# Optimization experiments

Hardware: AMD Instinct MI355X
Metric: run time of the kernel (lower is better)

The kernel has to match this reference:

```python
import math
import jax, jax.numpy as jnp
import numpy as np

B, T, C = 2, 2048, 1024
H, N1, N2, N3 = 16, 6, 4, 6
HD = C // H  # 64


def setup_inputs() -> dict:
    key = jax.random.key(0)
    k1, k2, k3 = jax.random.split(key, 3)
    return {
        "x": jax.random.normal(k1, (B, T, C), jnp.float32),
        "qkv_w": jax.random.normal(k2, (3 * C, C), jnp.float32) * (C ** -0.5),
        "proj_w": jax.random.normal(k3, (C, C), jnp.float32) * (C ** -0.5),
        "proj_b": jnp.zeros((C,), jnp.float32),
        "curvature": jnp.ones((1, N2, 1, 1), jnp.float32),
    }


def _rotary(T_, hd, dtype):
    inv_freq = 1.0 / (10000.0 ** (jnp.arange(0, hd, 2, dtype=jnp.float32) / hd))
    freqs = jnp.outer(jnp.arange(T_, dtype=jnp.float32), inv_freq)  # [T, hd/2]
    return jnp.cos(freqs)[None, :, None, :].astype(dtype), jnp.sin(freqs)[None, :, None, :].astype(dtype)


def _apply_rot(x, cos, sin):
    x1, x2 = x[..., : x.shape[-1] // 2], x[..., x.shape[-1] // 2 :]
    return jnp.concatenate([x1 * cos + x2 * sin, -x1 * sin + x2 * cos], axis=-1).astype(x.dtype)


def _causal_bias(L, S, dtype):
    mask = jnp.triu(jnp.ones((L, S), bool), k=1)
    return jnp.where(mask, jnp.asarray(-jnp.inf, dtype), jnp.asarray(0.0, dtype))


def _sdpa(q, k, v, scale):
    # q,k,v: [B,h,T,hd]
    scores = jnp.einsum("bhtd,bhsd->bhts", q, k) * scale + _causal_bias(q.shape[-2], k.shape[-2], q.dtype)
    return jnp.einsum("bhts,bhsd->bhtd", jax.nn.softmax(scores, axis=-1), v)


def _hyp_attn(q, k, v, curv):
    # Lorentz-model hyperbolic attention. project(x,k) = [sqrt(1/k+||x||^2), x];
    # d(u,v) = sqrt(1/k) * arccosh(-k * <u,v>_L), <u,v>_L = -u0 v0 + <u_s, v_s>.
    eps = 1e-6
    tq = jnp.sqrt(1.0 / curv + jnp.sum(q * q, axis=-1, keepdims=True))  # [B,h,T,1]
    tk = jnp.sqrt(1.0 / curv + jnp.sum(k * k, axis=-1, keepdims=True))  # [B,h,S,1]
    inner = jnp.einsum("bhtd,bhsd->bhts", q, k) - tq * jnp.swapaxes(tk, -1, -2)  # Lorentz inner [B,h,T,S]
    arg = jnp.maximum(-curv * inner, 1.0 + 1e-7)
    dis = jnp.sqrt(1.0 / curv) * jnp.arccosh(arg)
    scores = 1.0 / (eps + dis) + _causal_bias(q.shape[-2], k.shape[-2], q.dtype)
    return jnp.einsum("bhts,bhsd->bhtd", jax.nn.softmax(scores, axis=-1), v)


def reference(x, qkv_w, proj_w, proj_b, curvature):
    Bx, Tx, Cx = x.shape
    qkv = x @ qkv_w.T  # [B,T,3C]
    q, k, v = jnp.split(qkv, 3, axis=-1)
    q = q.reshape(Bx, Tx, H, HD)
    k = k.reshape(Bx, Tx, H, HD)
    v = v.reshape(Bx, Tx, H, HD)
    cos, sin = _rotary(Tx, HD, x.dtype)
    q = _apply_rot(q, cos, sin)
    k = _apply_rot(k, cos, sin)
    # -> [B,H,T,hd]
    q, k, v = (jnp.swapaxes(t, 1, 2) for t in (q, k, v))
    outs = []
    # euclidean heads
    outs.append(_sdpa(q[:, :N1], k[:, :N1], v[:, :N1], 1.0 / math.sqrt(HD)))
    # hyperbolic heads
    outs.append(_hyp_attn(q[:, N1 : N1 + N2], k[:, N1 : N1 + N2], v[:, N1 : N1 + N2], curvature))
    # spherical heads (cosine-sim attention, scale = sqrt(head_dim))
    qn = q[:, N1 + N2 :] / jnp.maximum(jnp.linalg.norm(q[:, N1 + N2 :], axis=-1, keepdims=True), 1e-12)
    kn = k[:, N1 + N2 :] / jnp.maximum(jnp.linalg.norm(k[:, N1 + N2 :], axis=-1, keepdims=True), 1e-12)
    outs.append(_sdpa(qn, kn, v[:, N1 + N2 :], math.sqrt(HD)))
    y = jnp.concatenate(outs, axis=1)  # [B,H,T,hd]
    y = jnp.swapaxes(y, 1, 2).reshape(Bx, Tx, Cx)
    return y @ proj_w.T + proj_b
```

## Files before the change

### kernel.cpp

```cpp
#include <hip/hip_runtime.h>
#include <stdint.h>
#include <math.h>


typedef __bf16 bf16x8 __attribute__((ext_vector_type(8)));
typedef float f32x4 __attribute__((ext_vector_type(4)));

static __device__ __forceinline__ float bf2f(unsigned short u) {
  union { unsigned int i; float f; } v; v.i = ((unsigned int)u) << 16; return v.f;
}
static __device__ __forceinline__ unsigned short f2bf(float f) {
  union { float f; unsigned int i; } v; v.f = f;
  unsigned int x = v.i;
  x += 0x7fffu + ((x >> 16) & 1u);
  return (unsigned short)(x >> 16);
}

static __device__ __forceinline__ void async_copy16(const void* gsrc, void* ldst) {
  auto* lp = reinterpret_cast<__attribute__((address_space(3))) unsigned int*>(
      reinterpret_cast<uintptr_t>(ldst));
  auto* gp = reinterpret_cast<const __attribute__((address_space(1))) unsigned int*>(
      reinterpret_cast<uintptr_t>(gsrc));
  __builtin_amdgcn_global_load_lds(gp, lp, 16, 0, 0);
}

template <int PAT>
__global__ __launch_bounds__(256) void split2(const float* __restrict__ in,
                                              unsigned short* __restrict__ out) {
  const int row = blockIdx.x;
  const int kq = threadIdx.x * 4;
  const f32x4 x = *(const f32x4*)(in + (size_t)row * 1024 + kq);
  unsigned short hi[4], lo[4];
#pragma unroll
  for (int i = 0; i < 4; ++i) {
    hi[i] = f2bf(x[i]);
    lo[i] = f2bf(x[i] - bf2f(hi[i]));
  }
  uint2 uh, ul;
  uh.x = (unsigned)hi[0] | ((unsigned)hi[1] << 16);
  uh.y = (unsigned)hi[2] | ((unsigned)hi[3] << 16);
  ul.x = (unsigned)lo[0] | ((unsigned)lo[1] << 16);
  ul.y = (unsigned)lo[2] | ((unsigned)lo[3] << 16);
  unsigned short* op = out + (size_t)row * 2048 + kq;
  *(uint2*)(op)        = uh;
  *(uint2*)(op + 1024) = PAT ? uh : ul;
}

__global__ __launch_bounds__(256) void split1(const float* __restrict__ in,
                                              unsigned short* __restrict__ out) {
  const int row = blockIdx.x;
  const int kq = threadIdx.x * 4;
  const f32x4 x = *(const f32x4*)(in + (size_t)row * 1024 + kq);
  uint2 uh;
  uh.x = (unsigned)f2bf(x[0]) | ((unsigned)f2bf(x[1]) << 16);
  uh.y = (unsigned)f2bf(x[2]) | ((unsigned)f2bf(x[3]) << 16);
  *(uint2*)(out + (size_t)row * 1024 + kq) = uh;
}

template <int HASBIAS>
__global__ __launch_bounds__(256) void gemm_bt2(
    const unsigned short* __restrict__ A, const unsigned short* __restrict__ Bm,
    float* __restrict__ C, const float* __restrict__ bias,
    int NX, int N_, int Kr, int loN) {
  alignas(16) __shared__ unsigned short smAh[128 * 64];
  alignas(16) __shared__ unsigned short smAl[128 * 64];
  alignas(16) __shared__ unsigned short smB [128 * 64];
  const int tid = threadIdx.x;
  const int lane = tid & 63;
  const int wvi = tid >> 6;
  const int wm = wvi >> 1, wn = wvi & 1;
  const int cpx = gridDim.x >> 3;
  const int wgid = ((int)blockIdx.x & 7) * cpx + ((int)blockIdx.x >> 3);
  const long m0 = (long)(wgid / NX) * 128, n0 = (long)(wgid % NX) * 128;
  const int K2w = Kr * 2;
  const bool skiplo = (n0 >= (long)loN);

  const f32x4 zero4 = {0.f, 0.f, 0.f, 0.f};
  f32x4 acc[4][4];
#pragma unroll
  for (int i = 0; i < 4; ++i)
#pragma unroll
    for (int j = 0; j < 4; ++j) acc[i][j] = zero4;

  int mrow[4], gg[4];
#pragma unroll
  for (int w = 0; w < 4; ++w) {
    int c = w * 256 + tid;
    mrow[w] = c >> 3;
    gg[w] = (c & 7) ^ ((c >> 3) & 7);
  }

  const int kTiles = Kr >> 6;
  for (int kt = 0; kt < kTiles; ++kt) {
    if (kt) __syncthreads();
    const int kb = kt << 6;
#pragma unroll
    for (int w = 0; w < 4; ++w) {
      const int c = w * 256 + tid;
      const size_t arow = (size_t)(m0 + mrow[w]) * K2w + kb + gg[w] * 8;
      async_copy16(A + arow,        (char*)smAh + c * 16);
      if (!skiplo)
        async_copy16(A + arow + Kr, (char*)smAl + c * 16);
      async_copy16(Bm + (size_t)(n0 + mrow[w]) * Kr + kb + gg[w] * 8,
                   (char*)smB + c * 16);
    }
    __syncthreads();
#pragma unroll
    for (int ks = 0; ks < 2; ++ks) {
      bf16x8 afh[4], afl[4], bg[4];
#pragma unroll
      for (int i = 0; i < 4; ++i) {
        const int ra = wm * 64 + i * 16 + (lane & 15);
        const int ga = (ks * 4 + (lane >> 4)) ^ (ra & 7);
        afh[i] = *(const bf16x8*)((const char*)smAh + ra * 128 + ga * 16);
        if (!skiplo)
          afl[i] = *(const bf16x8*)((const char*)smAl + ra * 128 + ga * 16);
        const int rb = wn * 64 + i * 16 + (lane & 15);
        const int gb2 = (ks * 4 + (lane >> 4)) ^ (rb & 7);
        bg[i] = *(const bf16x8*)((const char*)smB + rb * 128 + gb2 * 16);
      }
#pragma unroll
      for (int i = 0; i < 4; ++i)
#pragma unroll
        for (int j = 0; j < 4; ++j) {
          acc[i][j] = __builtin_amdgcn_mfma_f32_16x16x32_bf16(afh[i], bg[j], acc[i][j], 0, 0, 0);
          if (!skiplo)
            acc[i][j] = __builtin_amdgcn_mfma_f32_16x16x32_bf16(afl[i], bg[j], acc[i][j], 0, 0, 0);
        }
    }
  }

  const int r0 = wm * 64 + (lane >> 4) * 4;
  const int c0 = wn * 64 + (lane & 15);
#pragma unroll
  for (int j = 0; j < 4; ++j) {
    const long col = n0 + c0 + j * 16;
    float bv = 0.f;
    if (HASBIAS) bv = bias[col];
#pragma unroll
    for (int i = 0; i < 4; ++i) {
#pragma unroll
      for (int r = 0; r < 4; ++r) {
        const long row = m0 + r0 + i * 16 + r;
        C[row * N_ + col] = acc[i][j][r] + bv;
      }
    }
  }
}

__global__ __launch_bounds__(256) void prep(
    const float* __restrict__ qkvf, unsigned short* __restrict__ Q2,
    unsigned short* __restrict__ K2, unsigned short* __restrict__ V2,
    float* __restrict__ qq, float* __restrict__ kk, const float* __restrict__ curvg) {
  __shared__ unsigned short Vl[64 * 66];
  const int tid = threadIdx.x;
  const int zz = blockIdx.x;
  const int ttile = zz & 31, bh = zz >> 5;
  const int b = bh >> 4, h = bh & 15;
  const int t0 = ttile * 64;
  const int tr = tid >> 2, seg = tid & 3;
  const int t = t0 + tr;
  const float* src = qkvf + ((size_t)(b * 2048 + t)) * 3072 + h * 64 + seg * 16;

  float qv[16], kv[16], vv[16];
#pragma unroll
  for (int c = 0; c < 4; ++c) {
    const f32x4 a  = *(const f32x4*)(src + c * 4);
    const f32x4 bb = *(const f32x4*)(src + 1024 + c * 4);
    const f32x4 cc = *(const f32x4*)(src + 2048 + c * 4);
#pragma unroll
    for (int e = 0; e < 4; ++e) { qv[c*4+e] = a[e]; kv[c*4+e] = bb[e]; vv[c*4+e] = cc[e]; }
  }
  float qr[16], kr[16];
#pragma unroll
  for (int e = 0; e < 16; ++e) {
    const int d = seg * 16 + e;
    const int i = d & 31;
    const float invf = exp2f(-0.41524101186109286f * (float)i);
    float sn, cs;
    sincosf((float)t * invf, &sn, &cs);
    const float qo = __shfl_xor(qv[e], 2, 64);
    const float ko = __shfl_xor(kv[e], 2, 64);
    qr[e] = (d < 32) ? (qv[e] * cs + qo * sn) : (qv[e] * cs - qo * sn);
    kr[e] = (d < 32) ? (kv[e] * cs + ko * sn) : (kv[e] * cs - ko * sn);
  }
  float sq = 0.f, sk = 0.f;
#pragma unroll
  for (int e = 0; e < 16; ++e) { sq += qr[e] * qr[e]; sk += kr[e] * kr[e]; }
  sq += __shfl_xor(sq, 1, 64); sq += __shfl_xor(sq, 2, 64);
  sk += __shfl_xor(sk, 1, 64); sk += __shfl_xor(sk, 2, 64);
  float qscale = 0.125f * 1.4426950408889634f;
  if (h >= 10) {
    const float rq = 1.0f / fmaxf(sqrtf(sq), 1e-12f);
    const float rk = 1.0f / fmaxf(sqrtf(sk), 1e-12f);
#pragma unroll
    for (int e = 0; e < 16; ++e) { qr[e] *= rq; kr[e] *= rk; }
    qscale = 8.0f * 1.4426950408889634f;
  } else if (h >= 6) {
    qscale = 1.0f;
  }
#pragma unroll
  for (int e = 0; e < 16; ++e) qr[e] *= qscale;
  if (seg == 0) {
    const int idx = b * 32768 + h * 2048 + t;
    float oq = sq, ok = sk;
    if (h >= 6 && h < 10) {
      const float invc = 1.0f / curvg[h - 6];
      oq = sqrtf(invc + sq);
      ok = sqrtf(invc + sk);
    }
    qq[idx] = oq;
    kk[idx] = ok;
  }
  const int st = seg >> 1;
  const int quadA = (seg * 2) & 3, quadB = (seg * 2 + 1) & 3;
  {
    unsigned int wh[8], wl[8];
#pragma unroll
    for (int p = 0; p < 8; ++p) {
      unsigned short h0 = f2bf(qr[2*p]), h1 = f2bf(qr[2*p+1]);
      unsigned short l0 = f2bf(qr[2*p] - bf2f(h0)), l1 = f2bf(qr[2*p+1] - bf2f(h1));
      wh[p] = (unsigned)h0 | ((unsigned)h1 << 16);
      wl[p] = (unsigned)l0 | ((unsigned)l1 << 16);
    }
    const int qi = (t >> 4) & 1, c15q = t & 15;
    unsigned short* qs = Q2 + ((size_t)bh * 64 + (t >> 5)) * 4096;
    const int fh = ((qi * 2 + st) * 2 + 0) * 512, fl = fh + 512;
    *(uint4*)(qs + fh + quadA * 128 + c15q * 8) = uint4{wh[0], wh[1], wh[2], wh[3]};
    *(uint4*)(qs + fh + quadB * 128 + c15q * 8) = uint4{wh[4], wh[5], wh[6], wh[7]};
    *(uint4*)(qs + fl + quadA * 128 + c15q * 8) = uint4{wl[0], wl[1], wl[2], wl[3]};
    *(uint4*)(qs + fl + quadB * 128 + c15q * 8) = uint4{wl[4], wl[5], wl[6], wl[7]};
#pragma unroll
    for (int p = 0; p < 8; ++p) {
      unsigned short h0 = f2bf(kr[2*p]), h1 = f2bf(kr[2*p+1]);
      wh[p] = (unsigned)h0 | ((unsigned)h1 << 16);
    }
    const int kj = (tr >> 4) & 3, c15k = tr & 15;
    unsigned short* ks = K2 + ((size_t)bh * 32 + ttile) * 4096;
    const int gh = (st * 4 + kj) * 512;
    *(uint4*)(ks + gh + quadA * 128 + c15k * 8) = uint4{wh[0], wh[1], wh[2], wh[3]};
    *(uint4*)(ks + gh + quadB * 128 + c15k * 8) = uint4{wh[4], wh[5], wh[6], wh[7]};
  }
#pragma unroll
  for (int e = 0; e < 16; ++e) Vl[(seg * 16 + e) * 66 + tr] = f2bf(vv[e]);
  __syncthreads();
  {
    const int d = tid >> 2, tch = (tid & 3) * 16;
    unsigned int wv2[8];
#pragma unroll
    for (int p = 0; p < 8; ++p) {
      const unsigned short a0 = Vl[d * 66 + tch + 2*p];
      const unsigned short a1 = Vl[d * 66 + tch + 2*p + 1];
      wv2[p] = (unsigned)a0 | ((unsigned)a1 << 16);
    }
    const int dj = d >> 4, c15v = d & 15;
    const int ks2 = tch >> 5;
    const int qvA = (tch >> 3) & 3, qvB = ((tch >> 3) + 1) & 3;
    unsigned short* vs = V2 + ((size_t)bh * 32 + ttile) * 4096 + (ks2 * 4 + dj) * 512;
    *(uint4*)(vs + qvA * 128 + c15v * 8) = uint4{wv2[0], wv2[1], wv2[2], wv2[3]};
    *(uint4*)(vs + qvB * 128 + c15v * 8) = uint4{wv2[4], wv2[5], wv2[6], wv2[7]};
  }
}

__global__ __launch_bounds__(256, 2) void attn_part(
    const unsigned short* __restrict__ Q2, const unsigned short* __restrict__ K2,
    const unsigned short* __restrict__ V2, const float* __restrict__ tqq,
    const float* __restrict__ tkk, const float* __restrict__ curvg,
    float* __restrict__ part) {
  const int tid = threadIdx.x;
  const int lane = tid & 63;
  const int wv = tid >> 6;
  const int quad = lane >> 4, c15 = lane & 15;
  const int z = blockIdx.x * 4 + wv;
  const int bh = z / 160;
  const int u = 159 - (z - bh * 160);
  int qw, ch;
  if (u < 16)      { qw = u; ch = 0; }
  else if (u < 48) { qw = 16 + ((u - 16) >> 1); ch = (u - 16) & 1; }
  else if (u < 96) { const int s2 = u - 48; const int q3 = s2 / 3; qw = 32 + q3; ch = s2 - 3 * q3; }
  else             { const int s2 = u - 96; qw = 48 + (s2 >> 2); ch = s2 & 3; }
  const int h = bh & 15;
  const int geom = (h < 6) ? 0 : ((h < 10) ? 1 : 2);
  const int qrow0 = qw * 32;
  const f32x4 zero4 = {0.f, 0.f, 0.f, 0.f};

  const unsigned short* qbase = Q2 + ((size_t)bh * 64 + qw) * 4096;
  bf16x8 qh[2][2], ql[2][2];
#pragma unroll
  for (int qi = 0; qi < 2; ++qi)
#pragma unroll
    for (int st = 0; st < 2; ++st) {
      const int f = ((qi * 2 + st) * 2) * 512 + lane * 8;
      qh[qi][st] = *(const bf16x8*)(qbase + f);
      ql[qi][st] = *(const bf16x8*)(qbase + f + 512);
    }

  float curv = 1.f, sic = 1.f;
  const float Moff = 4.0f;
  float tqs[2] = {0.f, 0.f};
  if (geom == 1) {
    curv = curvg[h - 6];
    sic = sqrtf(1.0f / curv);
#pragma unroll
    for (int qi = 0; qi < 2; ++qi)
      tqs[qi] = tqq[bh * 2048 + qrow0 + qi * 16 + c15];
  }

  const __bf16 one_b = (__bf16)1.0f;
  const bf16x8 ones = {one_b, one_b, one_b, one_b, one_b, one_b, one_b, one_b};

  const int iA = ((quad & 1) * 32 + c15) * 4;
  const int iB = iA + 64;
  const bool hiq = (quad >= 2);

  f32x4 o[2][4];
  f32x4 ol[2] = {zero4, zero4};
#pragma unroll
  for (int qi = 0; qi < 2; ++qi)
#pragma unroll
    for (int dj = 0; dj < 4; ++dj) o[qi][dj] = zero4;

  const int nkt = (qw >> 1) + 1;
  const int ktB = ch * 8;
  const int ktE = (ktB + 8 < nkt) ? (ktB + 8) : nkt;
  for (int kt = ktB; kt < ktE; ++kt) {
    const int kb = kt * 64;
    const unsigned short* kbase = K2 + ((size_t)bh * 32 + kt) * 4096;
    const unsigned short* vbase = V2 + ((size_t)bh * 32 + kt) * 4096;

    bf16x8 kv[2][4];
#pragma unroll
    for (int st = 0; st < 2; ++st)
#pragma unroll
      for (int kj = 0; kj < 4; ++kj)
        kv[st][kj] = *(const bf16x8*)(kbase + (st * 4 + kj) * 512 + lane * 8);
    f32x4 tk4[4];
    if (geom == 1) {
#pragma unroll
      for (int kj = 0; kj < 4; ++kj)
        tk4[kj] = *(const f32x4*)(tkk + bh * 2048 + kb + kj * 16 + quad * 4);
    }

    f32x4 s[2][4];
#pragma unroll
    for (int qi = 0; qi < 2; ++qi)
#pragma unroll
      for (int kj = 0; kj < 4; ++kj) s[qi][kj] = zero4;
    __builtin_amdgcn_s_setprio(1);
#pragma unroll
    for (int st = 0; st < 2; ++st) {
#pragma unroll
      for (int kj = 0; kj < 4; ++kj) {
#pragma unroll
        for (int qi = 0; qi < 2; ++qi) {
          s[qi][kj] = __builtin_amdgcn_mfma_f32_16x16x32_bf16(kv[st][kj], qh[qi][st], s[qi][kj], 0, 0, 0);
          s[qi][kj] = __builtin_amdgcn_mfma_f32_16x16x32_bf16(kv[st][kj], ql[qi][st], s[qi][kj], 0, 0, 0);
        }
      }
    }
    __builtin_amdgcn_s_setprio(0);

#pragma unroll
    for (int ks2 = 0; ks2 < 2; ++ks2)
#pragma unroll
      for (int dj = 0; dj < 4; ++dj)
        kv[ks2][dj] = *(const bf16x8*)(vbase + (ks2 * 4 + dj) * 512 + lane * 8);

    const bool needmask = (kt == nkt - 1);
    unsigned pw[2][4][2];
#pragma unroll
    for (int qi = 0; qi < 2; ++qi) {
      const int qcol = qrow0 + qi * 16 + c15;
#pragma unroll
      for (int kj = 0; kj < 4; ++kj) {
        const int kloc = kb + kj * 16 + quad * 4;
        const f32x4 d4 = s[qi][kj];
        f32x4 p;
        if (geom == 1) {
          const float tq = tqs[qi];
#pragma unroll
          for (int r = 0; r < 4; ++r) {
            const float a = fmaxf(curv * (tq * tk4[kj][r] - d4[r]), 1.0f + 1e-7f);
            const float dis = sic * __logf(a + sqrtf(a * a - 1.0f));
            p[r] = __expf(__builtin_amdgcn_rcpf(1e-6f + dis) - Moff);
          }
        } else {
#pragma unroll
          for (int r = 0; r < 4; ++r) p[r] = exp2f(d4[r]);
        }
        if (needmask) {
#pragma unroll
          for (int r = 0; r < 4; ++r)
            if (kloc + r > qcol) p[r] = 0.0f;
        }
        union { float f; unsigned u2; } b0, b1, b2, b3;
        b0.f = p[0]; b1.f = p[1]; b2.f = p[2]; b3.f = p[3];
        pw[qi][kj][0] = (b0.u2 >> 16) | (b1.u2 & 0xffff0000u);
        pw[qi][kj][1] = (b2.u2 >> 16) | (b3.u2 & 0xffff0000u);
      }
    }

    __builtin_amdgcn_s_setprio(1);
#pragma unroll
    for (int ks2 = 0; ks2 < 2; ++ks2) {
      const int a = ks2 * 2, b2 = ks2 * 2 + 1;
#pragma unroll
      for (int qi = 0; qi < 2; ++qi) {
        const int w0A = __builtin_amdgcn_ds_bpermute(iA, (int)pw[qi][a][0]);
        const int w0B = __builtin_amdgcn_ds_bpermute(iA, (int)pw[qi][b2][0]);
        const int w1A = __builtin_amdgcn_ds_bpermute(iA, (int)pw[qi][a][1]);
        const int w1B = __builtin_amdgcn_ds_bpermute(iA, (int)pw[qi][b2][1]);
        const int w2A = __builtin_amdgcn_ds_bpermute(iB, (int)pw[qi][a][0]);
        const int w2B = __builtin_amdgcn_ds_bpermute(iB, (int)pw[qi][b2][0]);
        const int w3A = __builtin_amdgcn_ds_bpermute(iB, (int)pw[qi][a][1]);
        const int w3B = __builtin_amdgcn_ds_bpermute(iB, (int)pw[qi][b2][1]);
        union { uint4 u; bf16x8 v; } pf;
        pf.u.x = (unsigned)(hiq ? w0B : w0A);
        pf.u.y = (unsigned)(hiq ? w1B : w1A);
        pf.u.z = (unsigned)(hiq ? w2B : w2A);
        pf.u.w = (unsigned)(hiq ? w3B : w3A);
        const bf16x8 pfrag = pf.v;
        ol[qi] = __builtin_amdgcn_mfma_f32_16x16x32_bf16(ones, pfrag, ol[qi], 0, 0, 0);
#pragma unroll
        for (int dj = 0; dj < 4; ++dj)
          o[qi][dj] = __builtin_amdgcn_mfma_f32_16x16x32_bf16(kv[ks2][dj], pfrag, o[qi][dj], 0, 0, 0);
      }
    }
    __builtin_amdgcn_s_setprio(0);
  }

  float* slot = part + (size_t)(bh * 160 + u) * 2112;
#pragma unroll
  for (int qi = 0; qi < 2; ++qi)
#pragma unroll
    for (int dj = 0; dj < 4; ++dj)
      *(f32x4*)(slot + (qi * 4 + dj) * 256 + lane * 4) = o[qi][dj];
  if (quad == 0) {
#pragma unroll
    for (int qi = 0; qi < 2; ++qi)
      slot[2048 + qi * 16 + c15] = ol[qi][0];
  }
}

__global__ __launch_bounds__(256) void attn_reduce(
    const float* __restrict__ part, unsigned short* __restrict__ Ay) {
  __shared__ float Ol[4][32 * 65];
  const int tid = threadIdx.x;
  const int lane = tid & 63;
  const int wv = tid >> 6;
  float* Olw = &Ol[wv][0];
  const int quad = lane >> 4, c15 = lane & 15;
  const int z = blockIdx.x * 4 + wv, bh = z & 31, qw = 63 - (z >> 5);
  const int b = bh >> 4, h = bh & 15;
  const int G = qw >> 4;
  const int base = qw + 8 * G * (G - 1) + (qw & 15) * G;
  const float* slot0 = part + (size_t)(bh * 160 + base) * 2112;

  const f32x4 zero4 = {0.f, 0.f, 0.f, 0.f};
  f32x4 o[8];
  float ls[2] = {0.f, 0.f};
#pragma unroll
  for (int i = 0; i < 8; ++i) o[i] = zero4;
  for (int chv = 0; chv <= G; ++chv) {
    const float* sl = slot0 + chv * 2112;
#pragma unroll
    for (int i = 0; i < 8; ++i) o[i] += *(const f32x4*)(sl + i * 256 + lane * 4);
#pragma unroll
    for (int qi = 0; qi < 2; ++qi)
      ls[qi] += sl[2048 + qi * 16 + c15];
  }
#pragma unroll
  for (int qi = 0; qi < 2; ++qi) {
    const float invl = __builtin_amdgcn_rcpf(ls[qi]);
#pragma unroll
    for (int dj = 0; dj < 4; ++dj) {
      const f32x4 val = o[qi * 4 + dj] * invl;
#pragma unroll
      for (int r = 0; r < 4; ++r)
        Olw[(qi * 16 + c15) * 65 + dj * 16 + quad * 4 + r] = val[r];
    }
  }
  __syncthreads();
  const int row = lane >> 1, half = lane & 1;
  const float* rp = Olw + row * 65 + half * 32;
  unsigned int uh[16], ul2[16];
#pragma unroll
  for (int p = 0; p < 16; ++p) {
    const float v0 = rp[2 * p], v1 = rp[2 * p + 1];
    const unsigned short h0 = f2bf(v0), h1 = f2bf(v1);
    const unsigned short g0 = f2bf(v0 - bf2f(h0)), g1 = f2bf(v1 - bf2f(h1));
    uh[p] = (unsigned)h0 | ((unsigned)h1 << 16);
    ul2[p] = (unsigned)g0 | ((unsigned)g1 << 16);
  }
  unsigned short* yp = Ay + ((size_t)(b * 2048 + qw * 32 + row)) * 2048 + h * 64 + half * 32;
#pragma unroll
  for (int c = 0; c < 4; ++c) {
    *(uint4*)(yp + 8 * c)        = uint4{uh[4*c], uh[4*c+1], uh[4*c+2], uh[4*c+3]};
    *(uint4*)(yp + 1024 + 8 * c) = uint4{ul2[4*c], ul2[4*c+1], ul2[4*c+2], ul2[4*c+3]};
  }
}

extern "C" void kernel_launch(void* const* d_in, const int* in_sizes, int n_in,
                              void* d_out, int out_size, void* d_ws, size_t ws_size,
                              hipStream_t stream) {
  const float* x      = (const float*)d_in[0];
  const float* qkv_w  = (const float*)d_in[1];
  const float* proj_w = (const float*)d_in[2];
  const float* proj_b = (const float*)d_in[3];
  const float* curvature = (const float*)d_in[4];
  float* out = (float*)d_out;

  char* ws = (char*)d_ws;
  unsigned short* AX   = (unsigned short*)ws;
  unsigned short* BW1  = (unsigned short*)(ws + 16777216);
  float*          QKVF = (float*)(ws + 33554432);
  unsigned short* Q2   = (unsigned short*)ws;
  unsigned short* K2   = (unsigned short*)(ws + 16777216);
  unsigned short* V2   = (unsigned short*)(ws + 25165824);
  float*          PART = (float*)(ws + 33554432);
  unsigned short* BPW1 = (unsigned short*)(ws + 76808192);
  unsigned short* AY   = (unsigned short*)ws;
  float*          QQ   = (float*)(ws + 94371840);
  float*          KK   = (float*)(ws + 94633984);

  split2<0><<<4096, 256, 0, stream>>>(x, AX);
  split1<<<3072, 256, 0, stream>>>(qkv_w, BW1);

  gemm_bt2<0><<<768, 256, 0, stream>>>(AX, BW1, QKVF, nullptr, 24, 3072, 1024, 2048);

  prep<<<1024, 256, 0, stream>>>(QKVF, Q2, K2, V2, QQ, KK, curvature);

  split1<<<1024, 256, 0, stream>>>(proj_w, BPW1);

  attn_part<<<1280, 256, 0, stream>>>(Q2, K2, V2, QQ, KK, curvature, PART);

  attn_reduce<<<512, 256, 0, stream>>>(PART, AY);

  gemm_bt2<1><<<256, 256, 0, stream>>>(AY, BPW1, out, proj_b, 8, 1024, 1024, 1024);
}
```

Before: 264.0 us.

## Merge conversion kernels and rebalance causal attention split into paired halves

Fuses the three fp32-to-bf16 conversion launches into one kernel and moves the proj_w buffer so it is no longer overwritten by the attention partials. The attention work split changes from variable 8-tile chunks (160 work items per head) to 96 items per head. Query tiles 32-63 are split at key tile 16 into two pieces, and tiles 0-31 are handled whole, which evens out per-wave work. The reduce then sums at most two partials per row instead of up to four. Fewer partial writes and launches are traded for somewhat longer individual work items.

```diff
diff --git a/kernel.cpp b/kernel.cpp
--- a/kernel.cpp
+++ b/kernel.cpp
@@ -24,37 +24,40 @@
   __builtin_amdgcn_global_load_lds(gp, lp, 16, 0, 0);
 }
 
-template <int PAT>
-__global__ __launch_bounds__(256) void split2(const float* __restrict__ in,
-                                              unsigned short* __restrict__ out) {
-  const int row = blockIdx.x;
+__global__ __launch_bounds__(256) void split_all(
+    const float* __restrict__ x, const float* __restrict__ qkv_w,
+    const float* __restrict__ proj_w, unsigned short* __restrict__ AX,
+    unsigned short* __restrict__ BW1, unsigned short* __restrict__ BPW1) {
+  const int bid = blockIdx.x;
   const int kq = threadIdx.x * 4;
-  const f32x4 x = *(const f32x4*)(in + (size_t)row * 1024 + kq);
-  unsigned short hi[4], lo[4];
-#pragma unroll
-  for (int i = 0; i < 4; ++i) {
-    hi[i] = f2bf(x[i]);
-    lo[i] = f2bf(x[i] - bf2f(hi[i]));
-  }
-  uint2 uh, ul;
-  uh.x = (unsigned)hi[0] | ((unsigned)hi[1] << 16);
-  uh.y = (unsigned)hi[2] | ((unsigned)hi[3] << 16);
-  ul.x = (unsigned)lo[0] | ((unsigned)lo[1] << 16);
-  ul.y = (unsigned)lo[2] | ((unsigned)lo[3] << 16);
-  unsigned short* op = out + (size_t)row * 2048 + kq;
-  *(uint2*)(op)        = uh;
-  *(uint2*)(op + 1024) = PAT ? uh : ul;
-}
-
-__global__ __launch_bounds__(256) void split1(const float* __restrict__ in,
-                                              unsigned short* __restrict__ out) {
-  const int row = blockIdx.x;
-  const int kq = threadIdx.x * 4;
-  const f32x4 x = *(const f32x4*)(in + (size_t)row * 1024 + kq);
-  uint2 uh;
-  uh.x = (unsigned)f2bf(x[0]) | ((unsigned)f2bf(x[1]) << 16);
-  uh.y = (unsigned)f2bf(x[2]) | ((unsigned)f2bf(x[3]) << 16);
-  *(uint2*)(out + (size_t)row * 1024 + kq) = uh;
+  if (bid < 4096) {
+    const int row = bid;
+    const f32x4 v = *(const f32x4*)(x + (size_t)row * 1024 + kq);
+    unsigned short hi[4], lo[4];
+#pragma unroll
+    for (int i = 0; i < 4; ++i) {
+      hi[i] = f2bf(v[i]);
+      lo[i] = f2bf(v[i] - bf2f(hi[i]));
+    }
+    uint2 uh, ul;
+    uh.x = (unsigned)hi[0] | ((unsigned)hi[1] << 16);
+    uh.y = (unsigned)hi[2] | ((unsigned)hi[3] << 16);
+    ul.x = (unsigned)lo[0] | ((unsigned)lo[1] << 16);
+    ul.y = (unsigned)lo[2] | ((unsigned)lo[3] << 16);
+    unsigned short* op = AX + (size_t)row * 2048 + kq;
+    *(uint2*)(op)        = uh;
+    *(uint2*)(op + 1024) = ul;
+  } else {
+    const bool isq = (bid < 7168);
+    const int row = isq ? (bid - 4096) : (bid - 7168);
+    const float* src = isq ? qkv_w : proj_w;
+    unsigned short* dst = isq ? BW1 : BPW1;
+    const f32x4 v = *(const f32x4*)(src + (size_t)row * 1024 + kq);
+    uint2 uh;
+    uh.x = (unsigned)f2bf(v[0]) | ((unsigned)f2bf(v[1]) << 16);
+    uh.y = (unsigned)f2bf(v[2]) | ((unsigned)f2bf(v[3]) << 16);
+    *(uint2*)(dst + (size_t)row * 1024 + kq) = uh;
+  }
 }
 
 template <int HASBIAS>
@@ -272,13 +275,14 @@
   const int wv = tid >> 6;
   const int quad = lane >> 4, c15 = lane & 15;
   const int z = blockIdx.x * 4 + wv;
-  const int bh = z / 160;
-  const int u = 159 - (z - bh * 160);
-  int qw, ch;
-  if (u < 16)      { qw = u; ch = 0; }
-  else if (u < 48) { qw = 16 + ((u - 16) >> 1); ch = (u - 16) & 1; }
-  else if (u < 96) { const int s2 = u - 48; const int q3 = s2 / 3; qw = 32 + q3; ch = s2 - 3 * q3; }
-  else             { const int s2 = u - 96; qw = 48 + (s2 >> 2); ch = s2 & 3; }
+  const int u = z >> 5;
+  const int bh = z & 31;
+  int qw, ktB;
+  if (u < 32)      { qw = 32 + u;        ktB = 0;  }
+  else if (u < 64) { qw = 63 - (u - 32); ktB = 16; }
+  else             { qw = 31 - (u - 64); ktB = 0;  }
+  const int nkt = (qw >> 1) + 1;
+  const int ktE = (u < 32) ? 16 : nkt;
   const int h = bh & 15;
   const int geom = (h < 6) ? 0 : ((h < 10) ? 1 : 2);
   const int qrow0 = qw * 32;
@@ -320,9 +324,6 @@
 #pragma unroll
     for (int dj = 0; dj < 4; ++dj) o[qi][dj] = zero4;
 
-  const int nkt = (qw >> 1) + 1;
-  const int ktB = ch * 8;
-  const int ktE = (ktB + 8 < nkt) ? (ktB + 8) : nkt;
   for (int kt = ktB; kt < ktE; ++kt) {
     const int kb = kt * 64;
     const unsigned short* kbase = K2 + ((size_t)bh * 32 + kt) * 4096;
@@ -429,7 +430,7 @@
     __builtin_amdgcn_s_setprio(0);
   }
 
-  float* slot = part + (size_t)(bh * 160 + u) * 2112;
+  float* slot = part + (size_t)(bh * 96 + u) * 2112;
 #pragma unroll
   for (int qi = 0; qi < 2; ++qi)
 #pragma unroll
@@ -452,22 +453,25 @@
   const int quad = lane >> 4, c15 = lane & 15;
   const int z = blockIdx.x * 4 + wv, bh = z & 31, qw = 63 - (z >> 5);
   const int b = bh >> 4, h = bh & 15;
-  const int G = qw >> 4;
-  const int base = qw + 8 * G * (G - 1) + (qw & 15) * G;
-  const float* slot0 = part + (size_t)(bh * 160 + base) * 2112;
+  const int ua = (qw >= 32) ? (qw - 32) : (64 + (31 - qw));
+  const int ub = 32 + (63 - qw);
+  const float* slA = part + (size_t)(bh * 96 + ua) * 2112;
+  const float* slB = part + (size_t)(bh * 96 + ub) * 2112;
 
   const f32x4 zero4 = {0.f, 0.f, 0.f, 0.f};
   f32x4 o[8];
   float ls[2] = {0.f, 0.f};
 #pragma unroll
   for (int i = 0; i < 8; ++i) o[i] = zero4;
-  for (int chv = 0; chv <= G; ++chv) {
-    const float* sl = slot0 + chv * 2112;
-#pragma unroll
-    for (int i = 0; i < 8; ++i) o[i] += *(const f32x4*)(sl + i * 256 + lane * 4);
-#pragma unroll
-    for (int qi = 0; qi < 2; ++qi)
-      ls[qi] += sl[2048 + qi * 16 + c15];
+#pragma unroll
+  for (int i = 0; i < 8; ++i) o[i] += *(const f32x4*)(slA + i * 256 + lane * 4);
+#pragma unroll
+  for (int qi = 0; qi < 2; ++qi) ls[qi] += slA[2048 + qi * 16 + c15];
+  if (qw >= 32) {
+#pragma unroll
+    for (int i = 0; i < 8; ++i) o[i] += *(const f32x4*)(slB + i * 256 + lane * 4);
+#pragma unroll
+    for (int qi = 0; qi < 2; ++qi) ls[qi] += slB[2048 + qi * 16 + c15];
   }
 #pragma unroll
   for (int qi = 0; qi < 2; ++qi) {
@@ -514,25 +518,22 @@
   unsigned short* AX   = (unsigned short*)ws;
   unsigned short* BW1  = (unsigned short*)(ws + 16777216);
   float*          QKVF = (float*)(ws + 33554432);
+  unsigned short* BPW1 = (unsigned short*)(ws + 83886080);
   unsigned short* Q2   = (unsigned short*)ws;
   unsigned short* K2   = (unsigned short*)(ws + 16777216);
   unsigned short* V2   = (unsigned short*)(ws + 25165824);
   float*          PART = (float*)(ws + 33554432);
-  unsigned short* BPW1 = (unsigned short*)(ws + 76808192);
   unsigned short* AY   = (unsigned short*)ws;
   float*          QQ   = (float*)(ws + 94371840);
   float*          KK   = (float*)(ws + 94633984);
 
-  split2<0><<<4096, 256, 0, stream>>>(x, AX);
-  split1<<<3072, 256, 0, stream>>>(qkv_w, BW1);
+  split_all<<<8192, 256, 0, stream>>>(x, qkv_w, proj_w, AX, BW1, BPW1);
 
   gemm_bt2<0><<<768, 256, 0, stream>>>(AX, BW1, QKVF, nullptr, 24, 3072, 1024, 2048);
 
   prep<<<1024, 256, 0, stream>>>(QKVF, Q2, K2, V2, QQ, KK, curvature);
 
-  split1<<<1024, 256, 0, stream>>>(proj_w, BPW1);
-
-  attn_part<<<1280, 256, 0, stream>>>(Q2, K2, V2, QQ, KK, curvature, PART);
+  attn_part<<<768, 256, 0, stream>>>(Q2, K2, V2, QQ, KK, curvature, PART);
 
   attn_reduce<<<512, 256, 0, stream>>>(PART, AY);
 
```

Result: slower. 280.3 us (+6.2%).
